# Kernel optimization log

Measured on AMD Instinct MI355X. Metric: run time of the kernel, lower is better.

Reference implementation:

```python
import jax, jax.numpy as jnp
import numpy as np

N_HEAD = 16
ROPE_BASE = 10000.0


def _rope_tables(T, head_dim, dtype):
    # RotaryEmbedding(dim=head_dim//2): inv_freq over arange(0, dim, 2)/dim
    rot = head_dim // 2  # 32
    inv_freq = 1.0 / (ROPE_BASE ** (jnp.arange(0, rot, 2, dtype=jnp.float32) / rot))  # [rot/2]
    pos = jnp.arange(T, dtype=jnp.float32)
    freqs = jnp.outer(pos, inv_freq)                     # [T, rot/2]
    emb = jnp.concatenate([freqs, freqs], axis=-1)       # [T, rot]
    return jnp.cos(emb).astype(dtype), jnp.sin(emb).astype(dtype)


def _apply_rope(q, k, cos, sin):
    # q,k: [B,H,T,hd]; cos,sin: [T, hd//2] broadcast over B,H
    hd = q.shape[-1]
    half = hd // 2
    cos = cos[None, None]
    sin = sin[None, None]
    q1, q2 = q[..., :half], q[..., half:]
    k1, k2 = k[..., :half], k[..., half:]
    q_rot = jnp.concatenate([q1 * cos - q2 * sin, q2 * cos + q1 * sin], axis=-1)
    k_rot = jnp.concatenate([k1 * cos - k2 * sin, k2 * cos + k1 * sin], axis=-1)
    return q_rot, k_rot


def setup_inputs() -> dict:
    key = jax.random.key(0)
    ks = jax.random.split(key, 4)
    B, T, C = 4, 2048, 1024
    x = jax.random.normal(ks[0], (B, T, C), dtype=jnp.float32)
    W_attn = jax.random.normal(ks[1], (C, 3 * C), dtype=jnp.float32) * (1.0 / np.sqrt(C))
    b_attn = jnp.zeros((3 * C,), dtype=jnp.float32)
    W_proj = jax.random.normal(ks[2], (C, C), dtype=jnp.float32) * (1.0 / np.sqrt(C))
    b_proj = jnp.zeros((C,), dtype=jnp.float32)
    return {"x": x, "W_attn": W_attn, "b_attn": b_attn, "W_proj": W_proj, "b_proj": b_proj}


def reference(x, W_attn, b_attn, W_proj, b_proj):
    B, T, C = x.shape
    H = N_HEAD
    hd = C // H
    qkv = x @ W_attn + b_attn                            # [B,T,3C]
    q, k, v = jnp.split(qkv, 3, axis=-1)
    # [B,T,C] -> [B,H,T,hd]
    q = q.reshape(B, T, H, hd).transpose(0, 2, 1, 3)
    k = k.reshape(B, T, H, hd).transpose(0, 2, 1, 3)
    v = v.reshape(B, T, H, hd).transpose(0, 2, 1, 3)
    cos, sin = _rope_tables(T, hd, x.dtype)
    q, k = _apply_rope(q, k, cos, sin)
    att = jnp.einsum("bhqd,bhkd->bhqk", q, k) * (1.0 / np.sqrt(hd))
    causal = jnp.tril(jnp.ones((T, T), dtype=bool))
    att = jnp.where(causal[None, None], att, jnp.float32(-jnp.inf).astype(att.dtype))
    att = jax.nn.softmax(att, axis=-1)
    y = jnp.einsum("bhqk,bhkd->bhqd", att, v)            # [B,H,T,hd]
    y = y.transpose(0, 2, 1, 3).reshape(B, T, C)
    return y @ W_proj + b_proj
```

## Files before the change

kernel.cpp:

```cpp
#include <hip/hip_runtime.h>
#include <math.h>


typedef unsigned short u16;
typedef __bf16 bf16x8 __attribute__((ext_vector_type(8)));
typedef float f32x4 __attribute__((ext_vector_type(4)));
typedef float f32x16 __attribute__((ext_vector_type(16)));

#define QSCALE 0.18033688501389543f

__device__ __forceinline__ float b2f(u16 x) {
  union { unsigned u; float f; } c; c.u = ((unsigned)x) << 16; return c.f;
}
__device__ __forceinline__ u16 f2b(float f) {
  union { __bf16 h; u16 u; } c; c.h = (__bf16)f; return c.u;
}

#define GLOAD16(gp, lp)                                                  \
  __builtin_amdgcn_global_load_lds(                                      \
      (const __attribute__((address_space(1))) unsigned int*)(gp),       \
      (__attribute__((address_space(3))) unsigned int*)(lp), 16, 0, 0)

__global__ __launch_bounds__(256) void sentinel_k(u16* __restrict__ out, int n) {
  int i = blockIdx.x * 256 + threadIdx.x;
  if (i < n) out[i] = 0x4480;
}

__global__ __launch_bounds__(256) void transpose_f2b_k(const float* __restrict__ src,
                                                       u16* __restrict__ dst,
                                                       int R, int C) {
  __shared__ u16 tile[64][65];
  int tc = blockIdx.x * 64, tr = blockIdx.y * 64;
  int t = threadIdx.x;
  int rr = t >> 3;
  int c8 = (t & 7) * 8;
#pragma unroll
  for (int i = 0; i < 2; ++i) {
    int r = rr + i * 32;
    f32x4 p0 = *(const f32x4*)(src + (long)(tr + r) * C + tc + c8);
    f32x4 p1 = *(const f32x4*)(src + (long)(tr + r) * C + tc + c8 + 4);
#pragma unroll
    for (int j = 0; j < 4; ++j) {
      tile[r][c8 + j] = f2b(p0[j]);
      tile[r][c8 + 4 + j] = f2b(p1[j]);
    }
  }
  __syncthreads();
#pragma unroll
  for (int i = 0; i < 2; ++i) {
    int a = rr + i * 32;
    u16 vv[8];
#pragma unroll
    for (int j = 0; j < 8; ++j) vv[j] = tile[c8 + j][a];
    *(uint4*)(dst + (long)(tc + a) * R + tr + c8) = *(uint4*)vv;
  }
}

__global__ __launch_bounds__(256) void transpose_b_k(const u16* __restrict__ src,
                                                     u16* __restrict__ dst,
                                                     int R, int C,
                                                     long sBatch, long dBatch) {
  __shared__ u16 tile[64][65];
  src += (long)blockIdx.z * sBatch;
  dst += (long)blockIdx.z * dBatch;
  int tc = blockIdx.x * 64, tr = blockIdx.y * 64;
  int t = threadIdx.x;
  int rr = t >> 3;
  int c8 = (t & 7) * 8;
#pragma unroll
  for (int i = 0; i < 2; ++i) {
    int r = rr + i * 32;
    uint4 v = *(const uint4*)(src + (long)(tr + r) * C + tc + c8);
    u16 vv[8]; *(uint4*)vv = v;
#pragma unroll
    for (int j = 0; j < 8; ++j) tile[r][c8 + j] = vv[j];
  }
  __syncthreads();
#pragma unroll
  for (int i = 0; i < 2; ++i) {
    int a = rr + i * 32;
    u16 vv[8];
#pragma unroll
    for (int j = 0; j < 8; ++j) vv[j] = tile[c8 + j][a];
    *(uint4*)(dst + (long)(tc + a) * R + tr + c8) = *(uint4*)vv;
  }
}

__global__ void rope_table_k(float2* __restrict__ tab) {
  int i = blockIdx.x * 256 + threadIdx.x;
  if (i >= 2048 * 16) return;
  int t = i >> 4, f = i & 15;
  float invf = exp2f(-(float)f * (13.287712379549449f / 16.0f));
  float th = (float)t * invf;
  float s, c;
  sincosf(th, &s, &c);
  tab[i] = make_float2(c, s);
}

__global__ __launch_bounds__(256) void gemm_qkv_k(const float* __restrict__ A,
                                                  const u16* __restrict__ Bt,
                                                  const float* __restrict__ bias,
                                                  const float2* __restrict__ tab,
                                                  u16* __restrict__ out,
                                                  int M, int N, int K) {
  __shared__ u16 As[128 * 40];
  __shared__ u16 Bs[128 * 40];
  int tid = threadIdx.x, wid = tid >> 6, lane = tid & 63;
  int wr = wid >> 1, wc = wid & 1;
  long m0 = (long)blockIdx.x * 128, n0 = (long)blockIdx.y * 128;
  int r = lane & 15, g = lane >> 4;
  long arow = m0 + wid * 32 + (lane >> 2);
  int acol = (lane & 3) * 8;
  const float* Agf = A + arow * (long)K + acol;
  const u16* Bg = Bt + (n0 + wid * 32 + (lane >> 2)) * (long)K + acol;
  int lrow = wid * 32 + (lane >> 2);
  int lcol = acol;
  f32x4 acc[4][4] = {};
  int nk = K >> 5;
  for (int kt = 0; kt < nk; ++kt) {
    long ko = (long)kt * 32;
    f32x4 p0 = *(const f32x4*)(Agf + ko);
    f32x4 p1 = *(const f32x4*)(Agf + ko + 4);
    f32x4 p2 = *(const f32x4*)(Agf + ko + 16 * (long)K);
    f32x4 p3 = *(const f32x4*)(Agf + ko + 16 * (long)K + 4);
    u16 h0[8], h1[8];
#pragma unroll
    for (int j = 0; j < 4; ++j) {
      h0[j] = f2b(p0[j]); h0[4 + j] = f2b(p1[j]);
      h1[j] = f2b(p2[j]); h1[4 + j] = f2b(p3[j]);
    }
    uint4 a0 = *(uint4*)h0, a1 = *(uint4*)h1;
    uint4 b0 = *(const uint4*)(Bg + ko);
    uint4 b1 = *(const uint4*)(Bg + ko + 16 * (long)K);
    __syncthreads();
    *(uint4*)&As[lrow * 40 + lcol] = a0;
    *(uint4*)&As[(lrow + 16) * 40 + lcol] = a1;
    *(uint4*)&Bs[lrow * 40 + lcol] = b0;
    *(uint4*)&Bs[(lrow + 16) * 40 + lcol] = b1;
    __syncthreads();
    bf16x8 af[4], bfr[4];
#pragma unroll
    for (int mt = 0; mt < 4; ++mt)
      af[mt] = *(const bf16x8*)&As[(wr * 64 + mt * 16 + r) * 40 + g * 8];
#pragma unroll
    for (int nt = 0; nt < 4; ++nt)
      bfr[nt] = *(const bf16x8*)&Bs[(wc * 64 + nt * 16 + r) * 40 + g * 8];
#pragma unroll
    for (int mt = 0; mt < 4; ++mt)
#pragma unroll
      for (int nt = 0; nt < 4; ++nt)
        acc[mt][nt] = __builtin_amdgcn_mfma_f32_16x16x32_bf16(af[mt], bfr[nt], acc[mt][nt], 0, 0, 0);
  }
  int which = (int)(n0 >> 10);
  int hh = ((int)(n0 & 1023) >> 6) + wc;
  float bv[4];
#pragma unroll
  for (int nt = 0; nt < 4; ++nt) bv[nt] = bias[n0 + wc * 64 + nt * 16 + r];
#pragma unroll
  for (int mt = 0; mt < 4; ++mt) {
#pragma unroll
    for (int e = 0; e < 4; ++e) {
      long row = m0 + wr * 64 + mt * 16 + g * 4 + e;
      long bb = row >> 11;
      int tt = (int)row & 2047;
      float v0 = acc[mt][0][e] + bv[0];
      float v1 = acc[mt][1][e] + bv[1];
      float v2 = acc[mt][2][e] + bv[2];
      float v3 = acc[mt][3][e] + bv[3];
      if (which < 2) {
        float2 cs = tab[tt * 16 + r];
        float r0 = v0 * cs.x - v2 * cs.y, r2 = v2 * cs.x + v0 * cs.y;
        float r1 = v1 * cs.x - v3 * cs.y, r3 = v3 * cs.x + v1 * cs.y;
        if (which == 0) { r0 *= QSCALE; r1 *= QSCALE; r2 *= QSCALE; r3 *= QSCALE; }
        v0 = r0; v1 = r1; v2 = r2; v3 = r3;
      }
      u16* op = out + (long)which * 8388608 + (((bb * 16 + hh) * 2048 + tt) << 6);
      op[r] = f2b(v0);
      op[16 + r] = f2b(v1);
      op[32 + r] = f2b(v2);
      op[48 + r] = f2b(v3);
    }
  }
}

__global__ __launch_bounds__(256) void gemm_proj_k(const u16* __restrict__ A,
                                                   const u16* __restrict__ Bt,
                                                   const float* __restrict__ bias,
                                                   float* __restrict__ out,
                                                   int M, int N, int K) {
  __shared__ u16 As[128 * 32];
  __shared__ u16 Bs[128 * 32];
  int tid = threadIdx.x, wid = tid >> 6, lane = tid & 63;
  int wr = wid >> 1, wc = wid & 1;
  long m0 = (long)blockIdx.x * 128, n0 = (long)blockIdx.y * 128;
  int r = lane & 15, g = lane >> 4;
  const u16* Ag = A + (m0 + wid * 32 + (lane >> 2)) * (long)K + (lane & 3) * 8;
  const u16* Bg = Bt + (n0 + wid * 32 + (lane >> 2)) * (long)K + (lane & 3) * 8;
  u16* AsW = As + wid * 1024;
  u16* BsW = Bs + wid * 1024;
  f32x4 acc[4][4] = {};
  int nk = K >> 5;
  for (int kt = 0; kt < nk; ++kt) {
    long ko = (long)kt * 32;
    GLOAD16(Ag + ko, AsW);
    GLOAD16(Ag + ko + 16 * (long)K, AsW + 512);
    GLOAD16(Bg + ko, BsW);
    GLOAD16(Bg + ko + 16 * (long)K, BsW + 512);
    __syncthreads();
    bf16x8 af[4], bfr[4];
#pragma unroll
    for (int mt = 0; mt < 4; ++mt)
      af[mt] = *(const bf16x8*)&As[(wr * 64 + mt * 16 + r) * 32 + g * 8];
#pragma unroll
    for (int nt = 0; nt < 4; ++nt)
      bfr[nt] = *(const bf16x8*)&Bs[(wc * 64 + nt * 16 + r) * 32 + g * 8];
#pragma unroll
    for (int mt = 0; mt < 4; ++mt)
#pragma unroll
      for (int nt = 0; nt < 4; ++nt)
        acc[mt][nt] = __builtin_amdgcn_mfma_f32_16x16x32_bf16(af[mt], bfr[nt], acc[mt][nt], 0, 0, 0);
    __syncthreads();
  }
#pragma unroll
  for (int nt = 0; nt < 4; ++nt) {
    long col = n0 + wc * 64 + nt * 16 + r;
    float bvv = bias[col];
#pragma unroll
    for (int mt = 0; mt < 4; ++mt)
#pragma unroll
      for (int e = 0; e < 4; ++e) {
        long row = m0 + wr * 64 + mt * 16 + g * 4 + e;
        out[row * N + col] = acc[mt][nt][e] + bvv;
      }
  }
}

__global__ __launch_bounds__(256, 2) void attn_k(const u16* __restrict__ Qg,
                                                 const u16* __restrict__ Kg,
                                                 const u16* __restrict__ VgT,
                                                 u16* __restrict__ Y) {
  __shared__ u16 Ks[64 * 72];
  __shared__ u16 Vt[64 * 72];
  int ib = blockIdx.y;
  int bh = blockIdx.x;
  int b = bh >> 4, h = bh & 15;
  long base = (long)bh * (2048 * 64);
  int tid = threadIdx.x, wid = tid >> 6;
  int lane = tid & 63, l31 = lane & 31, hi = lane >> 5;
  int sA = ib * 4 + wid, sB = 63 - sA;
  int q0A = sA * 32, q0B = sB * 32;
  int endA = sA >> 1, endB = sB >> 1;
  int ktEnd = 31 - 2 * ib;
  bf16x8 qfA[4], qfB[4];
  {
    const u16* qa = Qg + base + (long)(q0A + l31) * 64 + hi * 8;
    const u16* qb = Qg + base + (long)(q0B + l31) * 64 + hi * 8;
#pragma unroll
    for (int s = 0; s < 4; ++s) {
      qfA[s] = *(const bf16x8*)(qa + s * 16);
      qfB[s] = *(const bf16x8*)(qb + s * 16);
    }
  }
  f32x16 accA0 = {}, accA1 = {}, accB0 = {}, accB1 = {};
  float mA = -INFINITY, lA = 0.f, mB = -INFINITY, lB = 0.f;
  for (int kt = 0; kt <= ktEnd; ++kt) {
    __syncthreads();
#pragma unroll
    for (int uu = 0; uu < 2; ++uu) {
      int u = tid + uu * 256;
      int row = u >> 3, c4 = (u & 7) * 8;
      *(uint4*)&Ks[row * 72 + c4] =
          *(const uint4*)&Kg[base + (long)(kt * 64 + row) * 64 + c4];
      *(uint4*)&Vt[row * 72 + c4] =
          *(const uint4*)&VgT[base + (long)row * 2048 + kt * 64 + c4];
    }
    __syncthreads();
    auto tileC = [&](const bf16x8 (&qf)[4], f32x16& acc0, f32x16& acc1,
                     float& mrow, float& lrow, int q0, int endS) {
      f32x16 st[2];
#pragma unroll
      for (int ct = 0; ct < 2; ++ct) {
        f32x16 z = {};
#pragma unroll
        for (int s = 0; s < 4; ++s) {
          bf16x8 kf = *(const bf16x8*)&Ks[(ct * 32 + l31) * 72 + s * 16 + hi * 8];
          z = __builtin_amdgcn_mfma_f32_32x32x16_bf16(kf, qf[s], z, 0, 0, 0);
        }
        st[ct] = z;
      }
      if (kt == endS) {
        int qg = q0 + l31;
#pragma unroll
        for (int ct = 0; ct < 2; ++ct)
#pragma unroll
          for (int reg = 0; reg < 16; ++reg) {
            int kg = kt * 64 + ct * 32 + (reg & 3) + 8 * (reg >> 2) + 4 * hi;
            if (kg > qg) st[ct][reg] = -INFINITY;
          }
      }
      float t8[8];
#pragma unroll
      for (int i = 0; i < 8; ++i)
        t8[i] = fmaxf(fmaxf(st[0][i], st[0][i + 8]), fmaxf(st[1][i], st[1][i + 8]));
#pragma unroll
      for (int i = 0; i < 4; ++i) t8[i] = fmaxf(t8[i], t8[i + 4]);
      float pm = fmaxf(fmaxf(t8[0], t8[1]), fmaxf(t8[2], t8[3]));
      pm = fmaxf(pm, __shfl_xor(pm, 32));
      if (__any(pm > mrow + 8.0f)) {
        float mn = fmaxf(mrow, pm);
        float alpha = exp2f(mrow - mn);
        mrow = mn;
        lrow *= alpha;
#pragma unroll
        for (int reg = 0; reg < 16; ++reg) {
          float aB = __shfl(alpha, (reg & 3) + 8 * (reg >> 2) + 4 * hi);
          acc0[reg] *= aB;
          acc1[reg] *= aB;
        }
      }
      float s8[8];
#pragma unroll
      for (int i = 0; i < 8; ++i) s8[i] = 0.f;
#pragma unroll
      for (int ct = 0; ct < 2; ++ct)
#pragma unroll
        for (int reg = 0; reg < 16; ++reg) {
          float p = exp2f(st[ct][reg] - mrow);
          st[ct][reg] = p;
          s8[reg & 7] += p;
        }
#pragma unroll
      for (int i = 0; i < 4; ++i) s8[i] += s8[i + 4];
      float rs = (s8[0] + s8[1]) + (s8[2] + s8[3]);
      rs += __shfl_xor(rs, 32);
      lrow += rs;
#pragma unroll
      for (int ct = 0; ct < 2; ++ct) {
        bf16x8 af[2];
#pragma unroll
        for (int ks = 0; ks < 2; ++ks) {
#pragma unroll
          for (int u = 0; u < 4; ++u) {
            float sendv = hi ? st[ct][8 * ks + u] : st[ct][8 * ks + 4 + u];
            float keepv = hi ? st[ct][8 * ks + 4 + u] : st[ct][8 * ks + u];
            float rcv = __shfl_xor(sendv, 32);
            af[ks][u] = (__bf16)(hi ? rcv : keepv);
            af[ks][4 + u] = (__bf16)(hi ? keepv : rcv);
          }
        }
#pragma unroll
        for (int ks = 0; ks < 2; ++ks) {
          bf16x8 vf0 = *(const bf16x8*)&Vt[l31 * 72 + ct * 32 + ks * 16 + hi * 8];
          bf16x8 vf1 = *(const bf16x8*)&Vt[(32 + l31) * 72 + ct * 32 + ks * 16 + hi * 8];
          acc0 = __builtin_amdgcn_mfma_f32_32x32x16_bf16(af[ks], vf0, acc0, 0, 0, 0);
          acc1 = __builtin_amdgcn_mfma_f32_32x32x16_bf16(af[ks], vf1, acc1, 0, 0, 0);
        }
      }
    };
    if (kt <= endA) tileC(qfA, accA0, accA1, mA, lA, q0A, endA);
    if (kt <= endB) tileC(qfB, accB0, accB1, mB, lB, q0B, endB);
  }
  auto writeO = [&](const f32x16& acc0, const f32x16& acc1, float lrow, int q0) {
    float rinv = 1.0f / lrow;
#pragma unroll
    for (int reg = 0; reg < 16; ++reg) {
      int crow = (reg & 3) + 8 * (reg >> 2) + 4 * hi;
      float rB = __shfl(rinv, crow);
      long orow = (long)(b * 2048 + q0 + crow) * 1024 + h * 64;
      Y[orow + l31] = f2b(acc0[reg] * rB);
      Y[orow + 32 + l31] = f2b(acc1[reg] * rB);
    }
  };
  writeO(accA0, accA1, lA, q0A);
  writeO(accB0, accB1, lB, q0B);
}

extern "C" void kernel_launch(void* const* d_in, const int* in_sizes, int n_in,
                              void* d_out, int out_size, void* d_ws, size_t ws_size,
                              hipStream_t stream) {
  const float* x  = (const float*)d_in[0];
  const float* Wa = (const float*)d_in[1];
  const float* ba = (const float*)d_in[2];
  const float* Wp = (const float*)d_in[3];
  const float* bp = (const float*)d_in[4];

  if (ws_size < 67108864ULL) {
    sentinel_k<<<dim3((out_size + 255) / 256), 256, 0, stream>>>((u16*)d_out, out_size);
    return;
  }

  u16* ws  = (u16*)d_ws;
  u16* Qg  = ws;
  u16* Kg  = ws + 8388608;
  u16* Vg  = ws + 16777216;
  u16* Yb  = ws + 16777216;
  u16* WaT = ws + 25165824;
  float2* tab = (float2*)(ws + 28311552);
  u16* VgT = ws + 25165824;
  u16* WpT = ws;

  transpose_f2b_k<<<dim3(48, 16), 256, 0, stream>>>(Wa, WaT, 1024, 3072);
  rope_table_k<<<dim3(128), 256, 0, stream>>>(tab);
  gemm_qkv_k<<<dim3(64, 24), 256, 0, stream>>>(x, WaT, ba, tab, Qg, 8192, 3072, 1024);
  transpose_b_k<<<dim3(1, 32, 64), 256, 0, stream>>>(Vg, VgT, 2048, 64, 131072L, 131072L);
  attn_k<<<dim3(64, 8), 256, 0, stream>>>(Qg, Kg, VgT, Yb);
  transpose_f2b_k<<<dim3(16, 16), 256, 0, stream>>>(Wp, WpT, 1024, 1024);
  gemm_proj_k<<<dim3(64, 8), 256, 0, stream>>>(Yb, WpT, bp, (float*)d_out, 8192, 1024, 1024);
}
```

Baseline: 211.2 us.

## Load 128-key tiles per barrier, interleave two query strips, use packed bf16 permlane exchange

The attention loop now stages 128 keys of K and V per synchronization instead of 64, which halves the number of barriers. Each 64-key sub-tile is processed for both query strips together, so each K/V LDS fragment read feeds two MFMAs. The P-matrix conversion now uses v_cvt_pk_bf16_f32 and v_permlane32_swap instead of per-element shuffles, which reduces cross-lane traffic. The trade-offs are more LDS per block, higher register pressure from the two interleaved strips, and a reliance on ktEnd+1 being even.

```diff
diff --git a/kernel.cpp b/kernel.cpp
--- a/kernel.cpp
+++ b/kernel.cpp
@@ -235,12 +235,127 @@
   }
 }
 
+__device__ __forceinline__ void pk_exchange(const f32x16& p, bf16x8& af0, bf16x8& af1) {
+  unsigned w0, w1, w2, w3, w4, w5, w6, w7;
+  asm("v_cvt_pk_bf16_f32 %0, %1, %2" : "=v"(w0) : "v"(p[0]), "v"(p[1]));
+  asm("v_cvt_pk_bf16_f32 %0, %1, %2" : "=v"(w1) : "v"(p[2]), "v"(p[3]));
+  asm("v_cvt_pk_bf16_f32 %0, %1, %2" : "=v"(w2) : "v"(p[4]), "v"(p[5]));
+  asm("v_cvt_pk_bf16_f32 %0, %1, %2" : "=v"(w3) : "v"(p[6]), "v"(p[7]));
+  asm("v_cvt_pk_bf16_f32 %0, %1, %2" : "=v"(w4) : "v"(p[8]), "v"(p[9]));
+  asm("v_cvt_pk_bf16_f32 %0, %1, %2" : "=v"(w5) : "v"(p[10]), "v"(p[11]));
+  asm("v_cvt_pk_bf16_f32 %0, %1, %2" : "=v"(w6) : "v"(p[12]), "v"(p[13]));
+  asm("v_cvt_pk_bf16_f32 %0, %1, %2" : "=v"(w7) : "v"(p[14]), "v"(p[15]));
+  asm("v_permlane32_swap_b32 %0, %1" : "+v"(w0), "+v"(w2));
+  asm("v_permlane32_swap_b32 %0, %1" : "+v"(w1), "+v"(w3));
+  asm("v_permlane32_swap_b32 %0, %1" : "+v"(w4), "+v"(w6));
+  asm("v_permlane32_swap_b32 %0, %1" : "+v"(w5), "+v"(w7));
+  union { unsigned u[4]; bf16x8 v; } c0, c1;
+  c0.u[0] = w0; c0.u[1] = w1; c0.u[2] = w2; c0.u[3] = w3;
+  c1.u[0] = w4; c1.u[1] = w5; c1.u[2] = w6; c1.u[3] = w7;
+  af0 = c0.v;
+  af1 = c1.v;
+}
+
+__device__ __forceinline__ void cmask(f32x16 (&st)[2], int kt, int q0, int l31, int hi) {
+  int qg = q0 + l31;
+#pragma unroll
+  for (int ct = 0; ct < 2; ++ct)
+#pragma unroll
+    for (int reg = 0; reg < 16; ++reg) {
+      int kg = kt * 64 + ct * 32 + (reg & 3) + 8 * (reg >> 2) + 4 * hi;
+      if (kg > qg) st[ct][reg] = -INFINITY;
+    }
+}
+
+__device__ __forceinline__ void online_sm(f32x16 (&st)[2], float& mrow, float& lrow,
+                                          f32x16& acc0, f32x16& acc1, int hi) {
+  float t8[8];
+#pragma unroll
+  for (int i = 0; i < 8; ++i)
+    t8[i] = fmaxf(fmaxf(st[0][i], st[0][i + 8]), fmaxf(st[1][i], st[1][i + 8]));
+#pragma unroll
+  for (int i = 0; i < 4; ++i) t8[i] = fmaxf(t8[i], t8[i + 4]);
+  float pm = fmaxf(fmaxf(t8[0], t8[1]), fmaxf(t8[2], t8[3]));
+  pm = fmaxf(pm, __shfl_xor(pm, 32));
+  if (__any(pm > mrow + 8.0f)) {
+    float mn = fmaxf(mrow, pm);
+    float alpha = exp2f(mrow - mn);
+    mrow = mn;
+    lrow *= alpha;
+#pragma unroll
+    for (int reg = 0; reg < 16; ++reg) {
+      float aB = __shfl(alpha, (reg & 3) + 8 * (reg >> 2) + 4 * hi);
+      acc0[reg] *= aB;
+      acc1[reg] *= aB;
+    }
+  }
+  float s8[8];
+#pragma unroll
+  for (int i = 0; i < 8; ++i) s8[i] = 0.f;
+#pragma unroll
+  for (int ct = 0; ct < 2; ++ct)
+#pragma unroll
+    for (int reg = 0; reg < 16; ++reg) {
+      float p = exp2f(st[ct][reg] - mrow);
+      st[ct][reg] = p;
+      s8[reg & 7] += p;
+    }
+#pragma unroll
+  for (int i = 0; i < 4; ++i) s8[i] += s8[i + 4];
+  float rs = (s8[0] + s8[1]) + (s8[2] + s8[3]);
+  rs += __shfl_xor(rs, 32);
+  lrow += rs;
+}
+
+template <bool WA>
+__device__ __forceinline__ void attn_tile(
+    const u16* __restrict__ Ks, const u16* __restrict__ Vt, int sub, int kt,
+    int l31, int hi, const bf16x8 (&qfA)[4], const bf16x8 (&qfB)[4],
+    f32x16& accA0, f32x16& accA1, f32x16& accB0, f32x16& accB1,
+    float& mA, float& lA, float& mB, float& lB,
+    int q0A, int q0B, int endA, int endB) {
+  f32x16 stA[2], stB[2];
+#pragma unroll
+  for (int ct = 0; ct < 2; ++ct) {
+    f32x16 zA = {}, zB = {};
+#pragma unroll
+    for (int s = 0; s < 4; ++s) {
+      bf16x8 kf = *(const bf16x8*)&Ks[(sub * 64 + ct * 32 + l31) * 72 + s * 16 + hi * 8];
+      if constexpr (WA) zA = __builtin_amdgcn_mfma_f32_32x32x16_bf16(kf, qfA[s], zA, 0, 0, 0);
+      zB = __builtin_amdgcn_mfma_f32_32x32x16_bf16(kf, qfB[s], zB, 0, 0, 0);
+    }
+    if constexpr (WA) stA[ct] = zA;
+    stB[ct] = zB;
+  }
+  if constexpr (WA) { if (kt == endA) cmask(stA, kt, q0A, l31, hi); }
+  if (kt == endB) cmask(stB, kt, q0B, l31, hi);
+  if constexpr (WA) online_sm(stA, mA, lA, accA0, accA1, hi);
+  online_sm(stB, mB, lB, accB0, accB1, hi);
+#pragma unroll
+  for (int ct = 0; ct < 2; ++ct) {
+    bf16x8 afA[2], afB[2];
+    if constexpr (WA) pk_exchange(stA[ct], afA[0], afA[1]);
+    pk_exchange(stB[ct], afB[0], afB[1]);
+#pragma unroll
+    for (int ks = 0; ks < 2; ++ks) {
+      bf16x8 vf0 = *(const bf16x8*)&Vt[l31 * 136 + sub * 64 + ct * 32 + ks * 16 + hi * 8];
+      bf16x8 vf1 = *(const bf16x8*)&Vt[(32 + l31) * 136 + sub * 64 + ct * 32 + ks * 16 + hi * 8];
+      if constexpr (WA) {
+        accA0 = __builtin_amdgcn_mfma_f32_32x32x16_bf16(afA[ks], vf0, accA0, 0, 0, 0);
+        accA1 = __builtin_amdgcn_mfma_f32_32x32x16_bf16(afA[ks], vf1, accA1, 0, 0, 0);
+      }
+      accB0 = __builtin_amdgcn_mfma_f32_32x32x16_bf16(afB[ks], vf0, accB0, 0, 0, 0);
+      accB1 = __builtin_amdgcn_mfma_f32_32x32x16_bf16(afB[ks], vf1, accB1, 0, 0, 0);
+    }
+  }
+}
+
 __global__ __launch_bounds__(256, 2) void attn_k(const u16* __restrict__ Qg,
                                                  const u16* __restrict__ Kg,
                                                  const u16* __restrict__ VgT,
                                                  u16* __restrict__ Y) {
-  __shared__ u16 Ks[64 * 72];
-  __shared__ u16 Vt[64 * 72];
+  __shared__ u16 Ks[128 * 72];
+  __shared__ u16 Vt[64 * 136];
   int ib = blockIdx.y;
   int bh = blockIdx.x;
   int b = bh >> 4, h = bh & 15;
@@ -263,102 +378,32 @@
   }
   f32x16 accA0 = {}, accA1 = {}, accB0 = {}, accB1 = {};
   float mA = -INFINITY, lA = 0.f, mB = -INFINITY, lB = 0.f;
-  for (int kt = 0; kt <= ktEnd; ++kt) {
-    __syncthreads();
-#pragma unroll
-    for (int uu = 0; uu < 2; ++uu) {
+  int pairs = (ktEnd + 1) >> 1;
+  for (int ktp = 0; ktp < pairs; ++ktp) {
+    __syncthreads();
+#pragma unroll
+    for (int uu = 0; uu < 4; ++uu) {
       int u = tid + uu * 256;
-      int row = u >> 3, c4 = (u & 7) * 8;
-      *(uint4*)&Ks[row * 72 + c4] =
-          *(const uint4*)&Kg[base + (long)(kt * 64 + row) * 64 + c4];
-      *(uint4*)&Vt[row * 72 + c4] =
-          *(const uint4*)&VgT[base + (long)row * 2048 + kt * 64 + c4];
-    }
-    __syncthreads();
-    auto tileC = [&](const bf16x8 (&qf)[4], f32x16& acc0, f32x16& acc1,
-                     float& mrow, float& lrow, int q0, int endS) {
-      f32x16 st[2];
-#pragma unroll
-      for (int ct = 0; ct < 2; ++ct) {
-        f32x16 z = {};
-#pragma unroll
-        for (int s = 0; s < 4; ++s) {
-          bf16x8 kf = *(const bf16x8*)&Ks[(ct * 32 + l31) * 72 + s * 16 + hi * 8];
-          z = __builtin_amdgcn_mfma_f32_32x32x16_bf16(kf, qf[s], z, 0, 0, 0);
-        }
-        st[ct] = z;
-      }
-      if (kt == endS) {
-        int qg = q0 + l31;
-#pragma unroll
-        for (int ct = 0; ct < 2; ++ct)
-#pragma unroll
-          for (int reg = 0; reg < 16; ++reg) {
-            int kg = kt * 64 + ct * 32 + (reg & 3) + 8 * (reg >> 2) + 4 * hi;
-            if (kg > qg) st[ct][reg] = -INFINITY;
-          }
-      }
-      float t8[8];
-#pragma unroll
-      for (int i = 0; i < 8; ++i)
-        t8[i] = fmaxf(fmaxf(st[0][i], st[0][i + 8]), fmaxf(st[1][i], st[1][i + 8]));
-#pragma unroll
-      for (int i = 0; i < 4; ++i) t8[i] = fmaxf(t8[i], t8[i + 4]);
-      float pm = fmaxf(fmaxf(t8[0], t8[1]), fmaxf(t8[2], t8[3]));
-      pm = fmaxf(pm, __shfl_xor(pm, 32));
-      if (__any(pm > mrow + 8.0f)) {
-        float mn = fmaxf(mrow, pm);
-        float alpha = exp2f(mrow - mn);
-        mrow = mn;
-        lrow *= alpha;
-#pragma unroll
-        for (int reg = 0; reg < 16; ++reg) {
-          float aB = __shfl(alpha, (reg & 3) + 8 * (reg >> 2) + 4 * hi);
-          acc0[reg] *= aB;
-          acc1[reg] *= aB;
-        }
-      }
-      float s8[8];
-#pragma unroll
-      for (int i = 0; i < 8; ++i) s8[i] = 0.f;
-#pragma unroll
-      for (int ct = 0; ct < 2; ++ct)
-#pragma unroll
-        for (int reg = 0; reg < 16; ++reg) {
-          float p = exp2f(st[ct][reg] - mrow);
-          st[ct][reg] = p;
-          s8[reg & 7] += p;
-        }
-#pragma unroll
-      for (int i = 0; i < 4; ++i) s8[i] += s8[i + 4];
-      float rs = (s8[0] + s8[1]) + (s8[2] + s8[3]);
-      rs += __shfl_xor(rs, 32);
-      lrow += rs;
-#pragma unroll
-      for (int ct = 0; ct < 2; ++ct) {
-        bf16x8 af[2];
-#pragma unroll
-        for (int ks = 0; ks < 2; ++ks) {
-#pragma unroll
-          for (int u = 0; u < 4; ++u) {
-            float sendv = hi ? st[ct][8 * ks + u] : st[ct][8 * ks + 4 + u];
-            float keepv = hi ? st[ct][8 * ks + 4 + u] : st[ct][8 * ks + u];
-            float rcv = __shfl_xor(sendv, 32);
-            af[ks][u] = (__bf16)(hi ? rcv : keepv);
-            af[ks][4 + u] = (__bf16)(hi ? keepv : rcv);
-          }
-        }
-#pragma unroll
-        for (int ks = 0; ks < 2; ++ks) {
-          bf16x8 vf0 = *(const bf16x8*)&Vt[l31 * 72 + ct * 32 + ks * 16 + hi * 8];
-          bf16x8 vf1 = *(const bf16x8*)&Vt[(32 + l31) * 72 + ct * 32 + ks * 16 + hi * 8];
-          acc0 = __builtin_amdgcn_mfma_f32_32x32x16_bf16(af[ks], vf0, acc0, 0, 0, 0);
-          acc1 = __builtin_amdgcn_mfma_f32_32x32x16_bf16(af[ks], vf1, acc1, 0, 0, 0);
-        }
-      }
-    };
-    if (kt <= endA) tileC(qfA, accA0, accA1, mA, lA, q0A, endA);
-    if (kt <= endB) tileC(qfB, accB0, accB1, mB, lB, q0B, endB);
+      int kr = u >> 3, kc = (u & 7) * 8;
+      *(uint4*)&Ks[kr * 72 + kc] =
+          *(const uint4*)&Kg[base + (long)(ktp * 128 + kr) * 64 + kc];
+      int vr = u >> 4, vc = (u & 15) * 8;
+      *(uint4*)&Vt[vr * 136 + vc] =
+          *(const uint4*)&VgT[base + (long)vr * 2048 + ktp * 128 + vc];
+    }
+    __syncthreads();
+#pragma unroll
+    for (int sub = 0; sub < 2; ++sub) {
+      int kt = ktp * 2 + sub;
+      if (kt <= endA)
+        attn_tile<true>(Ks, Vt, sub, kt, l31, hi, qfA, qfB,
+                        accA0, accA1, accB0, accB1, mA, lA, mB, lB,
+                        q0A, q0B, endA, endB);
+      else if (kt <= endB)
+        attn_tile<false>(Ks, Vt, sub, kt, l31, hi, qfA, qfB,
+                         accA0, accA1, accB0, accB1, mA, lA, mB, lB,
+                         q0A, q0B, endA, endB);
+    }
   }
   auto writeO = [&](const f32x16& acc0, const f32x16& acc1, float lrow, int q0) {
     float rinv = 1.0f / lrow;
```

Measured after the change: 214.4 us. No clear change (+1.5%).

## Read K/V directly from global in attention, one query strip per wave

Applied to the files above, without the earlier changes.

The attention kernel drops its LDS staging of K and V tiles and loads MFMA operands straight from global memory. Each wave now handles a single 32-row query strip instead of a balanced pair, the grid doubles to 16 query blocks launched heaviest-first, and occupancy rises to 4 blocks per CU. The softmax-to-bf16 conversion and cross-half exchange now use packed cvt plus permlane32 swap inline asm, and s_setprio is raised around the MFMA sections. Uncoalesced global reads of transposed V and the loss of the paired load balancing may offset the gains from removing LDS traffic and barriers.

```diff
diff --git a/kernel.cpp b/kernel.cpp
--- a/kernel.cpp
+++ b/kernel.cpp
@@ -235,144 +235,136 @@
   }
 }
 
-__global__ __launch_bounds__(256, 2) void attn_k(const u16* __restrict__ Qg,
+__device__ __forceinline__ void pk_exchange(const f32x16& p, bf16x8& af0, bf16x8& af1) {
+  unsigned w0, w1, w2, w3, w4, w5, w6, w7;
+  asm("v_cvt_pk_bf16_f32 %0, %1, %2" : "=v"(w0) : "v"(p[0]), "v"(p[1]));
+  asm("v_cvt_pk_bf16_f32 %0, %1, %2" : "=v"(w1) : "v"(p[2]), "v"(p[3]));
+  asm("v_cvt_pk_bf16_f32 %0, %1, %2" : "=v"(w2) : "v"(p[4]), "v"(p[5]));
+  asm("v_cvt_pk_bf16_f32 %0, %1, %2" : "=v"(w3) : "v"(p[6]), "v"(p[7]));
+  asm("v_cvt_pk_bf16_f32 %0, %1, %2" : "=v"(w4) : "v"(p[8]), "v"(p[9]));
+  asm("v_cvt_pk_bf16_f32 %0, %1, %2" : "=v"(w5) : "v"(p[10]), "v"(p[11]));
+  asm("v_cvt_pk_bf16_f32 %0, %1, %2" : "=v"(w6) : "v"(p[12]), "v"(p[13]));
+  asm("v_cvt_pk_bf16_f32 %0, %1, %2" : "=v"(w7) : "v"(p[14]), "v"(p[15]));
+  asm("v_permlane32_swap_b32 %0, %1" : "+v"(w0), "+v"(w2));
+  asm("v_permlane32_swap_b32 %0, %1" : "+v"(w1), "+v"(w3));
+  asm("v_permlane32_swap_b32 %0, %1" : "+v"(w4), "+v"(w6));
+  asm("v_permlane32_swap_b32 %0, %1" : "+v"(w5), "+v"(w7));
+  union { unsigned u[4]; bf16x8 v; } c0, c1;
+  c0.u[0] = w0; c0.u[1] = w1; c0.u[2] = w2; c0.u[3] = w3;
+  c1.u[0] = w4; c1.u[1] = w5; c1.u[2] = w6; c1.u[3] = w7;
+  af0 = c0.v;
+  af1 = c1.v;
+}
+
+__global__ __launch_bounds__(256, 4) void attn_k(const u16* __restrict__ Qg,
                                                  const u16* __restrict__ Kg,
                                                  const u16* __restrict__ VgT,
                                                  u16* __restrict__ Y) {
-  __shared__ u16 Ks[64 * 72];
-  __shared__ u16 Vt[64 * 72];
-  int ib = blockIdx.y;
+  int qb = 15 - (int)blockIdx.y;
   int bh = blockIdx.x;
   int b = bh >> 4, h = bh & 15;
   long base = (long)bh * (2048 * 64);
   int tid = threadIdx.x, wid = tid >> 6;
   int lane = tid & 63, l31 = lane & 31, hi = lane >> 5;
-  int sA = ib * 4 + wid, sB = 63 - sA;
-  int q0A = sA * 32, q0B = sB * 32;
-  int endA = sA >> 1, endB = sB >> 1;
-  int ktEnd = 31 - 2 * ib;
-  bf16x8 qfA[4], qfB[4];
+  int q0 = qb * 128 + wid * 32;
+  int endS = (q0 + 31) >> 6;
+  int ktMax = 2 * qb + 1;
+  bf16x8 qf[4];
   {
-    const u16* qa = Qg + base + (long)(q0A + l31) * 64 + hi * 8;
-    const u16* qb = Qg + base + (long)(q0B + l31) * 64 + hi * 8;
-#pragma unroll
-    for (int s = 0; s < 4; ++s) {
-      qfA[s] = *(const bf16x8*)(qa + s * 16);
-      qfB[s] = *(const bf16x8*)(qb + s * 16);
-    }
-  }
-  f32x16 accA0 = {}, accA1 = {}, accB0 = {}, accB1 = {};
-  float mA = -INFINITY, lA = 0.f, mB = -INFINITY, lB = 0.f;
-  for (int kt = 0; kt <= ktEnd; ++kt) {
+    const u16* qp = Qg + base + (long)(q0 + l31) * 64 + hi * 8;
+#pragma unroll
+    for (int s = 0; s < 4; ++s) qf[s] = *(const bf16x8*)(qp + s * 16);
+  }
+  f32x16 acc0 = {}, acc1 = {};
+  float mrow = -INFINITY, lrow = 0.f;
+  for (int kt = 0; kt <= ktMax; ++kt) {
     __syncthreads();
-#pragma unroll
-    for (int uu = 0; uu < 2; ++uu) {
-      int u = tid + uu * 256;
-      int row = u >> 3, c4 = (u & 7) * 8;
-      *(uint4*)&Ks[row * 72 + c4] =
-          *(const uint4*)&Kg[base + (long)(kt * 64 + row) * 64 + c4];
-      *(uint4*)&Vt[row * 72 + c4] =
-          *(const uint4*)&VgT[base + (long)row * 2048 + kt * 64 + c4];
-    }
-    __syncthreads();
-    auto tileC = [&](const bf16x8 (&qf)[4], f32x16& acc0, f32x16& acc1,
-                     float& mrow, float& lrow, int q0, int endS) {
-      f32x16 st[2];
-#pragma unroll
-      for (int ct = 0; ct < 2; ++ct) {
-        f32x16 z = {};
-#pragma unroll
-        for (int s = 0; s < 4; ++s) {
-          bf16x8 kf = *(const bf16x8*)&Ks[(ct * 32 + l31) * 72 + s * 16 + hi * 8];
-          z = __builtin_amdgcn_mfma_f32_32x32x16_bf16(kf, qf[s], z, 0, 0, 0);
+    if (kt > endS) continue;
+    const u16* kb = Kg + base + (long)(kt * 64) * 64;
+    f32x16 st[2];
+    __builtin_amdgcn_s_setprio(1);
+#pragma unroll
+    for (int ct = 0; ct < 2; ++ct) {
+      f32x16 z = {};
+#pragma unroll
+      for (int s = 0; s < 4; ++s) {
+        bf16x8 kf = *(const bf16x8*)&kb[(ct * 32 + l31) * 64 + s * 16 + hi * 8];
+        z = __builtin_amdgcn_mfma_f32_32x32x16_bf16(kf, qf[s], z, 0, 0, 0);
+      }
+      st[ct] = z;
+    }
+    __builtin_amdgcn_s_setprio(0);
+    if (kt == endS) {
+      int qg = q0 + l31;
+#pragma unroll
+      for (int ct = 0; ct < 2; ++ct)
+#pragma unroll
+        for (int reg = 0; reg < 16; ++reg) {
+          int kg = kt * 64 + ct * 32 + (reg & 3) + 8 * (reg >> 2) + 4 * hi;
+          if (kg > qg) st[ct][reg] = -INFINITY;
         }
-        st[ct] = z;
-      }
-      if (kt == endS) {
-        int qg = q0 + l31;
-#pragma unroll
-        for (int ct = 0; ct < 2; ++ct)
-#pragma unroll
-          for (int reg = 0; reg < 16; ++reg) {
-            int kg = kt * 64 + ct * 32 + (reg & 3) + 8 * (reg >> 2) + 4 * hi;
-            if (kg > qg) st[ct][reg] = -INFINITY;
-          }
-      }
-      float t8[8];
-#pragma unroll
-      for (int i = 0; i < 8; ++i)
-        t8[i] = fmaxf(fmaxf(st[0][i], st[0][i + 8]), fmaxf(st[1][i], st[1][i + 8]));
-#pragma unroll
-      for (int i = 0; i < 4; ++i) t8[i] = fmaxf(t8[i], t8[i + 4]);
-      float pm = fmaxf(fmaxf(t8[0], t8[1]), fmaxf(t8[2], t8[3]));
-      pm = fmaxf(pm, __shfl_xor(pm, 32));
-      if (__any(pm > mrow + 8.0f)) {
-        float mn = fmaxf(mrow, pm);
-        float alpha = exp2f(mrow - mn);
-        mrow = mn;
-        lrow *= alpha;
-#pragma unroll
-        for (int reg = 0; reg < 16; ++reg) {
-          float aB = __shfl(alpha, (reg & 3) + 8 * (reg >> 2) + 4 * hi);
-          acc0[reg] *= aB;
-          acc1[reg] *= aB;
-        }
-      }
-      float s8[8];
-#pragma unroll
-      for (int i = 0; i < 8; ++i) s8[i] = 0.f;
-#pragma unroll
-      for (int ct = 0; ct < 2; ++ct)
-#pragma unroll
-        for (int reg = 0; reg < 16; ++reg) {
-          float p = exp2f(st[ct][reg] - mrow);
-          st[ct][reg] = p;
-          s8[reg & 7] += p;
-        }
-#pragma unroll
-      for (int i = 0; i < 4; ++i) s8[i] += s8[i + 4];
-      float rs = (s8[0] + s8[1]) + (s8[2] + s8[3]);
-      rs += __shfl_xor(rs, 32);
-      lrow += rs;
-#pragma unroll
-      for (int ct = 0; ct < 2; ++ct) {
-        bf16x8 af[2];
-#pragma unroll
-        for (int ks = 0; ks < 2; ++ks) {
-#pragma unroll
-          for (int u = 0; u < 4; ++u) {
-            float sendv = hi ? st[ct][8 * ks + u] : st[ct][8 * ks + 4 + u];
-            float keepv = hi ? st[ct][8 * ks + 4 + u] : st[ct][8 * ks + u];
-            float rcv = __shfl_xor(sendv, 32);
-            af[ks][u] = (__bf16)(hi ? rcv : keepv);
-            af[ks][4 + u] = (__bf16)(hi ? keepv : rcv);
-          }
-        }
-#pragma unroll
-        for (int ks = 0; ks < 2; ++ks) {
-          bf16x8 vf0 = *(const bf16x8*)&Vt[l31 * 72 + ct * 32 + ks * 16 + hi * 8];
-          bf16x8 vf1 = *(const bf16x8*)&Vt[(32 + l31) * 72 + ct * 32 + ks * 16 + hi * 8];
-          acc0 = __builtin_amdgcn_mfma_f32_32x32x16_bf16(af[ks], vf0, acc0, 0, 0, 0);
-          acc1 = __builtin_amdgcn_mfma_f32_32x32x16_bf16(af[ks], vf1, acc1, 0, 0, 0);
-        }
-      }
-    };
-    if (kt <= endA) tileC(qfA, accA0, accA1, mA, lA, q0A, endA);
-    if (kt <= endB) tileC(qfB, accB0, accB1, mB, lB, q0B, endB);
-  }
-  auto writeO = [&](const f32x16& acc0, const f32x16& acc1, float lrow, int q0) {
-    float rinv = 1.0f / lrow;
-#pragma unroll
-    for (int reg = 0; reg < 16; ++reg) {
-      int crow = (reg & 3) + 8 * (reg >> 2) + 4 * hi;
-      float rB = __shfl(rinv, crow);
-      long orow = (long)(b * 2048 + q0 + crow) * 1024 + h * 64;
-      Y[orow + l31] = f2b(acc0[reg] * rB);
-      Y[orow + 32 + l31] = f2b(acc1[reg] * rB);
-    }
-  };
-  writeO(accA0, accA1, lA, q0A);
-  writeO(accB0, accB1, lB, q0B);
+    }
+    float t8[8];
+#pragma unroll
+    for (int i = 0; i < 8; ++i)
+      t8[i] = fmaxf(fmaxf(st[0][i], st[0][i + 8]), fmaxf(st[1][i], st[1][i + 8]));
+#pragma unroll
+    for (int i = 0; i < 4; ++i) t8[i] = fmaxf(t8[i], t8[i + 4]);
+    float pm = fmaxf(fmaxf(t8[0], t8[1]), fmaxf(t8[2], t8[3]));
+    pm = fmaxf(pm, __shfl_xor(pm, 32));
+    if (__any(pm > mrow + 8.0f)) {
+      float mn = fmaxf(mrow, pm);
+      float alpha = exp2f(mrow - mn);
+      mrow = mn;
+      lrow *= alpha;
+#pragma unroll
+      for (int reg = 0; reg < 16; ++reg) {
+        float aB = __shfl(alpha, (reg & 3) + 8 * (reg >> 2) + 4 * hi);
+        acc0[reg] *= aB;
+        acc1[reg] *= aB;
+      }
+    }
+    float s8[8];
+#pragma unroll
+    for (int i = 0; i < 8; ++i) s8[i] = 0.f;
+#pragma unroll
+    for (int ct = 0; ct < 2; ++ct)
+#pragma unroll
+      for (int reg = 0; reg < 16; ++reg) {
+        float p = exp2f(st[ct][reg] - mrow);
+        st[ct][reg] = p;
+        s8[reg & 7] += p;
+      }
+#pragma unroll
+    for (int i = 0; i < 4; ++i) s8[i] += s8[i + 4];
+    float rs = (s8[0] + s8[1]) + (s8[2] + s8[3]);
+    rs += __shfl_xor(rs, 32);
+    lrow += rs;
+#pragma unroll
+    for (int ct = 0; ct < 2; ++ct) {
+      bf16x8 af[2];
+      pk_exchange(st[ct], af[0], af[1]);
+      const u16* vb = VgT + base + kt * 64 + ct * 32;
+      __builtin_amdgcn_s_setprio(1);
+#pragma unroll
+      for (int ks = 0; ks < 2; ++ks) {
+        bf16x8 vf0 = *(const bf16x8*)&vb[(long)l31 * 2048 + ks * 16 + hi * 8];
+        bf16x8 vf1 = *(const bf16x8*)&vb[(long)(32 + l31) * 2048 + ks * 16 + hi * 8];
+        acc0 = __builtin_amdgcn_mfma_f32_32x32x16_bf16(af[ks], vf0, acc0, 0, 0, 0);
+        acc1 = __builtin_amdgcn_mfma_f32_32x32x16_bf16(af[ks], vf1, acc1, 0, 0, 0);
+      }
+      __builtin_amdgcn_s_setprio(0);
+    }
+  }
+  float rinv = 1.0f / lrow;
+#pragma unroll
+  for (int reg = 0; reg < 16; ++reg) {
+    int crow = (reg & 3) + 8 * (reg >> 2) + 4 * hi;
+    float rB = __shfl(rinv, crow);
+    long orow = (long)(b * 2048 + q0 + crow) * 1024 + h * 64;
+    Y[orow + l31] = f2b(acc0[reg] * rB);
+    Y[orow + 32 + l31] = f2b(acc1[reg] * rB);
+  }
 }
 
 extern "C" void kernel_launch(void* const* d_in, const int* in_sizes, int n_in,
@@ -403,7 +395,7 @@
   rope_table_k<<<dim3(128), 256, 0, stream>>>(tab);
   gemm_qkv_k<<<dim3(64, 24), 256, 0, stream>>>(x, WaT, ba, tab, Qg, 8192, 3072, 1024);
   transpose_b_k<<<dim3(1, 32, 64), 256, 0, stream>>>(Vg, VgT, 2048, 64, 131072L, 131072L);
-  attn_k<<<dim3(64, 8), 256, 0, stream>>>(Qg, Kg, VgT, Yb);
+  attn_k<<<dim3(64, 16), 256, 0, stream>>>(Qg, Kg, VgT, Yb);
   transpose_f2b_k<<<dim3(16, 16), 256, 0, stream>>>(Wp, WpT, 1024, 1024);
   gemm_proj_k<<<dim3(64, 8), 256, 0, stream>>>(Yb, WpT, bp, (float*)d_out, 8192, 1024, 1024);
 }
```

After: 283.7 us (median of 2 runs). 1.34x slower.
